# Performance work log

Measured on AMD Instinct MI355X. Metric: run time of the kernel, lower is better.

## Reference

```python
import jax, jax.numpy as jnp
import numpy as np

EMB = 64
N_LEFT = 100000   # m: rows of left_features, b
N_RIGHT = 100000  # n: rows of right_features, c
N_EDGES = 3200000


def setup_inputs() -> dict:
    key = jax.random.key(0)
    ks = jax.random.split(key, 12)
    inp = {
        "left_features": jax.random.normal(ks[0], (N_LEFT, EMB), jnp.float32),
        "right_features_k": jax.random.normal(ks[1], (N_RIGHT, EMB), jnp.float32),
        "edge_index": jax.random.randint(ks[2], (N_EDGES, 2), 0, N_RIGHT, jnp.int64),
        "edge_weight": jax.random.uniform(ks[3], (N_EDGES,), jnp.float32),
        "right_features": jax.random.normal(ks[4], (N_RIGHT, EMB), jnp.float32),
        "c": jax.random.normal(ks[5], (N_RIGHT, 1), jnp.float32),
        "b": jax.random.normal(ks[6], (N_LEFT, 1), jnp.float32),
        # learned parameters
        "temp": jnp.full((2,), 0.9, jnp.float32),
        "W1": jax.random.normal(ks[7], (EMB, EMB), jnp.float32) * 0.05,
        "b1": jnp.zeros((EMB,), jnp.float32),
        "W2": jax.random.normal(ks[8], (EMB, EMB), jnp.float32) * 0.05,
        "b2": jnp.zeros((EMB,), jnp.float32),
    }
    return inp


def reference(left_features, right_features_k, edge_index, edge_weight,
              right_features, c, b, temp, W1, b1, W2, b2):
    # right_to_left=False branch of BipartiteGraphConvolution.forward
    n = right_features.shape[0]  # = c.shape[0]
    # Source quirk: values.sum(dim=-1) on a 1-D vector is a GLOBAL scalar sum,
    # clamped to min 1; every edge weight is scaled by 1/that scalar.
    total = jnp.maximum(jnp.sum(edge_weight), 1.0)
    vals = edge_weight / total                                    # [E]
    row = edge_index[:, 0]  # destination (right) node, in [0, n)
    col = edge_index[:, 1]  # source (left) node, in [0, m)
    # sparse-dense matmul: conv_output = A @ left_features, A in COO (coalesce
    # just sums duplicate entries, identical to segment-sum over raw edges)
    msg = left_features[col] * vals[:, None]                      # [E, EMB]
    conv_output = jax.ops.segment_sum(msg, row, num_segments=n)   # [n, EMB]
    h = right_features + temp[1] * (c - conv_output)              # [n, EMB]
    # output_module: Linear -> ReLU -> Linear (torch Linear: x @ W.T + b)
    h = jax.nn.relu(h @ W1.T + b1)
    out = h @ W2.T + b2
    return out
```

## Files before the change

kernel.cpp:

```cpp
#include <hip/hip_runtime.h>

#define EMB 64
#define BROWS 512
#define BSHIFT 9
#define CHUNK 4096
#define COLBITS 23
#define COLMASK ((1u << COLBITS) - 1u)

__device__ __forceinline__ unsigned short f2bf(float f) {
    unsigned u = __float_as_uint(f);
    u = u + 0x7FFFu + ((u >> 16) & 1u);
    return (unsigned short)(u >> 16);
}

__global__ void convert_left_kernel(const float* __restrict__ left,
                                    unsigned* __restrict__ left16, int n2) {
    int i = blockIdx.x * blockDim.x + threadIdx.x;
    if (i >= n2) return;
    float2 v = ((const float2*)left)[i];
    left16[i] = (unsigned)f2bf(v.x) | ((unsigned)f2bf(v.y) << 16);
}

__global__ void init_bcur_kernel(int* __restrict__ bcur, int nb, int slot) {
    int t = threadIdx.x;
    if (t < nb) bcur[t] = t * slot;
}

__global__ __launch_bounds__(256) void partition_kernel(
    const int2* __restrict__ eidx, const float* __restrict__ w, int n_edges,
    int* __restrict__ bcursor, int2* __restrict__ bsorted,
    float* __restrict__ total) {
    __shared__ int lh[256];
    __shared__ int lo[256];
    __shared__ int go[256];
    __shared__ int lcur[256];
    __shared__ int2 stage[CHUNK];
    __shared__ int dstg[CHUNK];
    int t = threadIdx.x;
    int base = blockIdx.x * CHUNK;
    int cnt = min(CHUNK, n_edges - base);

    lh[t] = 0;
    __syncthreads();
    #pragma unroll
    for (int k = 0; k < CHUNK / 256; ++k) {
        int e = base + t + k * 256;
        if (e < n_edges) atomicAdd(&lh[eidx[e].x >> BSHIFT], 1);
    }
    __syncthreads();
    int v = lh[t];
    lo[t] = v;
    __syncthreads();
    for (int off = 1; off < 256; off <<= 1) {
        int u = (t >= off) ? lo[t - off] : 0;
        __syncthreads();
        lo[t] += u;
        __syncthreads();
    }
    int excl = lo[t] - v;
    go[t] = (v > 0) ? atomicAdd(&bcursor[t], v) : 0;
    __syncthreads();
    lo[t] = excl;
    lcur[t] = excl;
    __syncthreads();

    float s = 0.f;
    #pragma unroll
    for (int k = 0; k < CHUNK / 256; ++k) {
        int e = base + t + k * 256;
        if (e < n_edges) {
            int2 rc = eidx[e];
            float wv = w[e];
            s += wv;
            int b = rc.x >> BSHIFT;
            unsigned rl = (unsigned)(rc.x & (BROWS - 1));
            int p = atomicAdd(&lcur[b], 1);
            stage[p] = make_int2((int)((rl << COLBITS) | (unsigned)rc.y),
                                 __float_as_int(wv));
            dstg[p] = go[b] + (p - lo[b]);
        }
    }
    #pragma unroll
    for (int off = 32; off > 0; off >>= 1) s += __shfl_down(s, off, 64);
    if ((t & 63) == 0) atomicAdd(total, s);
    __syncthreads();
    #pragma unroll
    for (int k = 0; k < CHUNK / 256; ++k) {
        int s2 = t + k * 256;
        if (s2 < cnt) bsorted[dstg[s2]] = stage[s2];
    }
}

__global__ __launch_bounds__(256, 1) void count_scan_kernel(
    const int* __restrict__ bcur, int* __restrict__ sbase, int nb, int slot) {
    __shared__ int ssc[256];
    int t = threadIdx.x;
    int cnt = (t < nb) ? (bcur[t] - t * slot) : 0;
    ssc[t] = cnt;
    __syncthreads();
    for (int off = 1; off < 256; off <<= 1) {
        int u = (t >= off) ? ssc[t - off] : 0;
        __syncthreads();
        ssc[t] += u;
        __syncthreads();
    }
    if (t < nb) sbase[t] = ssc[t] - cnt;
}

__global__ __launch_bounds__(256) void local_rowsort_kernel(
    const int2* __restrict__ bsorted, const int* __restrict__ bcur,
    const int* __restrict__ sbase, int* __restrict__ offs,
    int2* __restrict__ sorted2, int n_right, int slot) {
    __shared__ int lhist[BROWS];
    __shared__ int lcur[BROWS];
    __shared__ int ps[256];
    int b = blockIdx.x;
    int t = threadIdx.x;
    int src0 = b * slot;
    int send = min(bcur[b], src0 + slot);
    int dbase = sbase[b];
    int row0 = b << BSHIFT;
    int nrows = min(BROWS, n_right - row0);

    lhist[2 * t] = 0;
    lhist[2 * t + 1] = 0;
    __syncthreads();
    for (int e = src0 + t; e < send; e += 256)
        atomicAdd(&lhist[((unsigned)bsorted[e].x) >> COLBITS], 1);
    __syncthreads();

    int v0 = lhist[2 * t];
    int v1 = lhist[2 * t + 1];
    int pv = v0 + v1;
    ps[t] = pv;
    __syncthreads();
    for (int off = 1; off < 256; off <<= 1) {
        int u = (t >= off) ? ps[t - off] : 0;
        __syncthreads();
        ps[t] += u;
        __syncthreads();
    }
    int epair = ps[t] - pv;
    lcur[2 * t] = epair;
    lcur[2 * t + 1] = epair + v0;
    if (2 * t < nrows)     offs[row0 + 2 * t]     = dbase + epair;
    if (2 * t + 1 < nrows) offs[row0 + 2 * t + 1] = dbase + epair + v0;
    __syncthreads();

    int e = src0 + t;
    for (; e + 3 * 256 < send; e += 4 * 256) {
        int2 e0 = bsorted[e + 0 * 256];
        int2 e1 = bsorted[e + 1 * 256];
        int2 e2 = bsorted[e + 2 * 256];
        int2 e3 = bsorted[e + 3 * 256];
        int p0 = atomicAdd(&lcur[((unsigned)e0.x) >> COLBITS], 1);
        int p1 = atomicAdd(&lcur[((unsigned)e1.x) >> COLBITS], 1);
        int p2 = atomicAdd(&lcur[((unsigned)e2.x) >> COLBITS], 1);
        int p3 = atomicAdd(&lcur[((unsigned)e3.x) >> COLBITS], 1);
        sorted2[dbase + p0] = e0;
        sorted2[dbase + p1] = e1;
        sorted2[dbase + p2] = e2;
        sorted2[dbase + p3] = e3;
    }
    for (; e < send; e += 256) {
        int2 e0 = bsorted[e];
        int p0 = atomicAdd(&lcur[((unsigned)e0.x) >> COLBITS], 1);
        sorted2[dbase + p0] = e0;
    }
}

__global__ void seg_gather_bf16_kernel(const int2* __restrict__ sorted,
                                       const int* __restrict__ offs,
                                       const uint4* __restrict__ left16o,
                                       const float* __restrict__ right,
                                       const float* __restrict__ c,
                                       const float* __restrict__ temp,
                                       const float* __restrict__ total,
                                       float* __restrict__ hout, int n_right,
                                       int n_edges, int offs_are_ends) {
    int gid = blockIdx.x * blockDim.x + threadIdx.x;
    int wid = gid >> 6;
    int lane = gid & 63;
    if (wid >= n_right) return;
    int start, end;
    if (offs_are_ends) {
        end = offs[wid];
        start = (wid == 0) ? 0 : offs[wid - 1];
    } else {
        start = offs[wid];
        end = (wid + 1 < n_right) ? offs[wid + 1] : n_edges;
    }

    int sub = lane >> 3;
    int d8  = lane & 7;

    float cv = c[wid];
    float inv = 1.0f / fmaxf(total[0], 1.0f);
    float t1 = temp[1];

    float a0 = 0.f, a1 = 0.f, a2 = 0.f, a3 = 0.f;
    float a4 = 0.f, a5 = 0.f, a6 = 0.f, a7 = 0.f;

    if (start < end) {
        int ee = start + sub;
        int2 sv = sorted[(ee < end) ? ee : (end - 1)];
        for (int base = start; base < end; base += 8) {
            int2 cur = sv;
            int ecur = base + sub;
            int bnext = base + 8;
            if (bnext < end) {
                int en = bnext + sub;
                sv = sorted[(en < end) ? en : (end - 1)];
            }
            float wv = (ecur < end) ? __int_as_float(cur.y) : 0.f;
            unsigned col = (unsigned)cur.x & COLMASK;
            uint4 pk = left16o[(size_t)col * 8 + d8];
            a0 = fmaf(wv, __uint_as_float(pk.x << 16), a0);
            a1 = fmaf(wv, __uint_as_float(pk.x & 0xffff0000u), a1);
            a2 = fmaf(wv, __uint_as_float(pk.y << 16), a2);
            a3 = fmaf(wv, __uint_as_float(pk.y & 0xffff0000u), a3);
            a4 = fmaf(wv, __uint_as_float(pk.z << 16), a4);
            a5 = fmaf(wv, __uint_as_float(pk.z & 0xffff0000u), a5);
            a6 = fmaf(wv, __uint_as_float(pk.w << 16), a6);
            a7 = fmaf(wv, __uint_as_float(pk.w & 0xffff0000u), a7);
        }
    }

    #define RED8(x) x += __shfl_xor(x, 8, 64); x += __shfl_xor(x, 16, 64); \
                    x += __shfl_xor(x, 32, 64);
    RED8(a0) RED8(a1) RED8(a2) RED8(a3) RED8(a4) RED8(a5) RED8(a6) RED8(a7)
    #undef RED8

    if (lane < 8) {
        const float4* rp = (const float4*)(right + (size_t)wid * EMB);
        float4 r0 = rp[2 * lane];
        float4 r1 = rp[2 * lane + 1];
        float4 h0, h1;
        h0.x = r0.x + t1 * (cv - a0 * inv);
        h0.y = r0.y + t1 * (cv - a1 * inv);
        h0.z = r0.z + t1 * (cv - a2 * inv);
        h0.w = r0.w + t1 * (cv - a3 * inv);
        h1.x = r1.x + t1 * (cv - a4 * inv);
        h1.y = r1.y + t1 * (cv - a5 * inv);
        h1.z = r1.z + t1 * (cv - a6 * inv);
        h1.w = r1.w + t1 * (cv - a7 * inv);
        float4* op = (float4*)(hout + (size_t)wid * EMB);
        op[2 * lane] = h0;
        op[2 * lane + 1] = h1;
    }
}

__global__ __launch_bounds__(256, 1) void mlp_kernel(
    const float* __restrict__ W1, const float* __restrict__ b1,
    const float* __restrict__ W2, const float* __restrict__ b2,
    float* __restrict__ io, int n) {
    int r = blockIdx.x * blockDim.x + threadIdx.x;
    if (r >= n) return;

    float h[EMB];
    const float4* qp = (const float4*)(io + (size_t)r * EMB);
    #pragma unroll
    for (int q = 0; q < EMB / 4; ++q) {
        float4 qv = qp[q];
        h[4 * q + 0] = qv.x;
        h[4 * q + 1] = qv.y;
        h[4 * q + 2] = qv.z;
        h[4 * q + 3] = qv.w;
    }

    float h1[EMB];
    #pragma unroll
    for (int j = 0; j < EMB; j += 4) {
        float s0 = b1[j + 0], s1 = b1[j + 1], s2 = b1[j + 2], s3 = b1[j + 3];
        #pragma unroll
        for (int k = 0; k < EMB; ++k) {
            float hk = h[k];
            s0 = fmaf(hk, W1[(j + 0) * EMB + k], s0);
            s1 = fmaf(hk, W1[(j + 1) * EMB + k], s1);
            s2 = fmaf(hk, W1[(j + 2) * EMB + k], s2);
            s3 = fmaf(hk, W1[(j + 3) * EMB + k], s3);
        }
        h1[j + 0] = fmaxf(s0, 0.f);
        h1[j + 1] = fmaxf(s1, 0.f);
        h1[j + 2] = fmaxf(s2, 0.f);
        h1[j + 3] = fmaxf(s3, 0.f);
    }

    float4* op = (float4*)(io + (size_t)r * EMB);
    #pragma unroll
    for (int j = 0; j < EMB; j += 4) {
        float s0 = b2[j + 0], s1 = b2[j + 1], s2 = b2[j + 2], s3 = b2[j + 3];
        #pragma unroll
        for (int k = 0; k < EMB; ++k) {
            float hk = h1[k];
            s0 = fmaf(hk, W2[(j + 0) * EMB + k], s0);
            s1 = fmaf(hk, W2[(j + 1) * EMB + k], s1);
            s2 = fmaf(hk, W2[(j + 2) * EMB + k], s2);
            s3 = fmaf(hk, W2[(j + 3) * EMB + k], s3);
        }
        op[j / 4] = make_float4(s0, s1, s2, s3);
    }
}


__global__ void hist_total_kernel(const int2* __restrict__ eidx,
                                  const float* __restrict__ w, int n_edges,
                                  int* __restrict__ counts,
                                  float* __restrict__ total) {
    int gid = blockIdx.x * blockDim.x + threadIdx.x;
    int stride = gridDim.x * blockDim.x;
    float s = 0.f;
    for (int e = gid; e < n_edges; e += stride) {
        s += w[e];
        atomicAdd(&counts[eidx[e].x], 1);
    }
    #pragma unroll
    for (int off = 32; off > 0; off >>= 1) s += __shfl_down(s, off, 64);
    if ((threadIdx.x & 63) == 0) atomicAdd(total, s);
}

__global__ __launch_bounds__(1024, 1) void scan1_kernel(
    const int* __restrict__ cnt, int* __restrict__ incl,
    int* __restrict__ bsums, int n) {
    __shared__ int s[1024];
    int t = threadIdx.x;
    int i = blockIdx.x * 1024 + t;
    int v = (i < n) ? cnt[i] : 0;
    s[t] = v;
    __syncthreads();
    for (int off = 1; off < 1024; off <<= 1) {
        int u = (t >= off) ? s[t - off] : 0;
        __syncthreads();
        s[t] += u;
        __syncthreads();
    }
    if (i < n) incl[i] = s[t];
    if (t == 1023) bsums[blockIdx.x] = s[t];
}

__global__ __launch_bounds__(256, 1) void scan2_kernel(int* __restrict__ bsums, int nb) {
    __shared__ int s[256];
    int t = threadIdx.x;
    int v = (t < nb) ? bsums[t] : 0;
    s[t] = v;
    __syncthreads();
    for (int off = 1; off < 256; off <<= 1) {
        int u = (t >= off) ? s[t - off] : 0;
        __syncthreads();
        s[t] += u;
        __syncthreads();
    }
    if (t < nb) bsums[t] = s[t] - v;
}

__global__ void scan3_kernel(const int* __restrict__ incl,
                             const int* __restrict__ base,
                             int* __restrict__ offs, int n) {
    int i = blockIdx.x * blockDim.x + threadIdx.x;
    if (i >= n) return;
    offs[i] = (i == 0) ? 0 : incl[i - 1] + base[(i - 1) >> 10];
}

__global__ void scatter_kernel(const int2* __restrict__ eidx,
                               const float* __restrict__ w, int n_edges,
                               int* __restrict__ offs,
                               int2* __restrict__ sorted) {
    int gid = blockIdx.x * blockDim.x + threadIdx.x;
    int stride = gridDim.x * blockDim.x;
    for (int e = gid; e < n_edges; e += stride) {
        int2 rc = eidx[e];
        float v = w[e];
        int pos = atomicAdd(&offs[rc.x], 1);
        sorted[pos] = make_int2(rc.y, __float_as_int(v));
    }
}


__global__ void sum_weights_kernel(const float* __restrict__ w, int n,
                                   float* __restrict__ total) {
    int gid = blockIdx.x * blockDim.x + threadIdx.x;
    int stride = gridDim.x * blockDim.x;
    float s = 0.f;
    for (int i = gid; i < n; i += stride) s += w[i];
    #pragma unroll
    for (int off = 32; off > 0; off >>= 1) s += __shfl_down(s, off, 64);
    if ((threadIdx.x & 63) == 0) atomicAdd(total, s);
}

__global__ void edge_scatter_kernel(const int* __restrict__ idx,
                                    const float* __restrict__ w,
                                    const float* __restrict__ left,
                                    const float* __restrict__ total,
                                    float* __restrict__ conv,
                                    long long n_threads) {
    long long gid = (long long)blockIdx.x * blockDim.x + threadIdx.x;
    if (gid >= n_threads) return;
    int e = (int)(gid >> 6);
    int d = (int)(gid & 63);
    float inv = 1.0f / fmaxf(total[0], 1.0f);
    int row = idx[2 * e];
    int col = idx[2 * e + 1];
    float v = w[e] * inv;
    float msg = left[(size_t)col * EMB + d] * v;
    atomicAdd(&conv[(size_t)row * EMB + d], msg);
}

__global__ __launch_bounds__(256, 1) void fused_mlp_kernel(
    const float* __restrict__ right, const float* __restrict__ c,
    const float* __restrict__ temp,
    const float* __restrict__ W1, const float* __restrict__ b1,
    const float* __restrict__ W2, const float* __restrict__ b2,
    float* __restrict__ io, int n) {
    int r = blockIdx.x * blockDim.x + threadIdx.x;
    if (r >= n) return;
    float t1 = temp[1];
    float cv = c[r];
    float h[EMB];
    const float4* rp = (const float4*)(right + (size_t)r * EMB);
    const float4* qp = (const float4*)(io + (size_t)r * EMB);
    #pragma unroll
    for (int q = 0; q < EMB / 4; ++q) {
        float4 rv = rp[q];
        float4 qv = qp[q];
        h[4 * q + 0] = rv.x + t1 * (cv - qv.x);
        h[4 * q + 1] = rv.y + t1 * (cv - qv.y);
        h[4 * q + 2] = rv.z + t1 * (cv - qv.z);
        h[4 * q + 3] = rv.w + t1 * (cv - qv.w);
    }
    float h1[EMB];
    #pragma unroll
    for (int j = 0; j < EMB; j += 4) {
        float s0 = b1[j], s1 = b1[j + 1], s2 = b1[j + 2], s3 = b1[j + 3];
        #pragma unroll
        for (int k = 0; k < EMB; ++k) {
            float hk = h[k];
            s0 = fmaf(hk, W1[(j + 0) * EMB + k], s0);
            s1 = fmaf(hk, W1[(j + 1) * EMB + k], s1);
            s2 = fmaf(hk, W1[(j + 2) * EMB + k], s2);
            s3 = fmaf(hk, W1[(j + 3) * EMB + k], s3);
        }
        h1[j] = fmaxf(s0, 0.f);
        h1[j + 1] = fmaxf(s1, 0.f);
        h1[j + 2] = fmaxf(s2, 0.f);
        h1[j + 3] = fmaxf(s3, 0.f);
    }
    float4* op = (float4*)(io + (size_t)r * EMB);
    #pragma unroll
    for (int j = 0; j < EMB; j += 4) {
        float s0 = b2[j], s1 = b2[j + 1], s2 = b2[j + 2], s3 = b2[j + 3];
        #pragma unroll
        for (int k = 0; k < EMB; ++k) {
            float hk = h1[k];
            s0 = fmaf(hk, W2[(j + 0) * EMB + k], s0);
            s1 = fmaf(hk, W2[(j + 1) * EMB + k], s1);
            s2 = fmaf(hk, W2[(j + 2) * EMB + k], s2);
            s3 = fmaf(hk, W2[(j + 3) * EMB + k], s3);
        }
        op[j / 4] = make_float4(s0, s1, s2, s3);
    }
}


extern "C" void kernel_launch(void* const* d_in, const int* in_sizes, int n_in,
                              void* d_out, int out_size, void* d_ws, size_t ws_size,
                              hipStream_t stream) {
    const float* left   = (const float*)d_in[0];
    const int*   eidx   = (const int*)d_in[2];
    const float* ew     = (const float*)d_in[3];
    const float* right  = (const float*)d_in[4];
    const float* c      = (const float*)d_in[5];
    const float* temp   = (const float*)d_in[7];
    const float* W1     = (const float*)d_in[8];
    const float* b1     = (const float*)d_in[9];
    const float* W2     = (const float*)d_in[10];
    const float* b2     = (const float*)d_in[11];

    const int n_edges = in_sizes[3];
    const int n_right = in_sizes[4] / EMB;
    const int n_left  = in_sizes[0] / EMB;
    float* out = (float*)d_out;

    const int nb = (n_right + BROWS - 1) >> BSHIFT;
    const int nblocks_scan = (n_right + 1023) / 1024;

    auto align256 = [](size_t x) { return (x + 255) & ~(size_t)255; };

    int slot = n_edges / (nb > 0 ? nb : 1);
    slot += slot / 16 + 128;

    size_t off_bcur    = 64;
    size_t off_sbase   = align256(off_bcur + (size_t)nb * 4);
    size_t off_offs    = align256(off_sbase + (size_t)(nb + 1) * 4);
    size_t off_bsorted = align256(off_offs + (size_t)n_right * 4);
    size_t off_sorted2 = align256(off_bsorted + ((size_t)nb * slot + slot) * 8);
    size_t off_left16f = align256(off_sorted2 + (size_t)n_edges * 8);
    size_t req_full    = off_left16f + (size_t)n_left * EMB * 2;

    size_t m_off_offs   = 64;
    size_t m_off_incl   = align256(m_off_offs + (size_t)n_right * 4);
    size_t m_off_bsum   = align256(m_off_incl + (size_t)n_right * 4);
    size_t m_off_sorted = align256(m_off_bsum + 1024);
    size_t m_off_left16 = align256(m_off_sorted + (size_t)n_edges * 8);
    size_t req_mid      = m_off_left16 + (size_t)n_left * EMB * 2;

    bool common_ok = (nb <= 256) && (nblocks_scan <= 256) &&
                     (n_left <= (1 << COLBITS)) && (BROWS * nb >= n_right);

    if (common_ok && ws_size >= req_full) {
        char* ws = (char*)d_ws;
        float* total = (float*)ws;
        int* bcur = (int*)(ws + off_bcur);
        int* sbase = (int*)(ws + off_sbase);
        int* offs = (int*)(ws + off_offs);
        int2* bsorted = (int2*)(ws + off_bsorted);
        int2* sorted2 = (int2*)(ws + off_sorted2);
        unsigned short* left16 = (unsigned short*)(ws + off_left16f);

        hipMemsetAsync(ws, 0, 64, stream);

        int n2 = n_left * EMB / 2;
        convert_left_kernel<<<(n2 + 255) / 256, 256, 0, stream>>>(
            left, (unsigned*)left16, n2);
        init_bcur_kernel<<<1, 256, 0, stream>>>(bcur, nb, slot);
        {
            int nchunks = (n_edges + CHUNK - 1) / CHUNK;
            partition_kernel<<<nchunks, 256, 0, stream>>>(
                (const int2*)eidx, ew, n_edges, bcur, bsorted, total);
        }
        count_scan_kernel<<<1, 256, 0, stream>>>(bcur, sbase, nb, slot);
        local_rowsort_kernel<<<nb, 256, 0, stream>>>(bsorted, bcur, sbase, offs,
                                                     sorted2, n_right, slot);
        {
            long long n_threads = (long long)n_right * EMB;
            int blocks = (int)((n_threads + 255) / 256);
            seg_gather_bf16_kernel<<<blocks, 256, 0, stream>>>(
                sorted2, offs, (const uint4*)left16, right, c, temp, total,
                out, n_right, n_edges, 0);
        }
        mlp_kernel<<<(n_right + 255) / 256, 256, 0, stream>>>(W1, b1, W2, b2,
                                                              out, n_right);
    } else if (common_ok && ws_size >= req_mid) {
        char* ws = (char*)d_ws;
        float* total = (float*)ws;
        int* offs = (int*)(ws + m_off_offs);
        int* incl = (int*)(ws + m_off_incl);
        int* bsum = (int*)(ws + m_off_bsum);
        int2* sorted = (int2*)(ws + m_off_sorted);
        unsigned short* left16 = (unsigned short*)(ws + m_off_left16);

        hipMemsetAsync(ws, 0, m_off_offs + (size_t)n_right * 4, stream);

        int n2 = n_left * EMB / 2;
        convert_left_kernel<<<(n2 + 255) / 256, 256, 0, stream>>>(
            left, (unsigned*)left16, n2);
        hist_total_kernel<<<2048, 256, 0, stream>>>((const int2*)eidx, ew,
                                                    n_edges, offs, total);
        scan1_kernel<<<nblocks_scan, 1024, 0, stream>>>(offs, incl, bsum, n_right);
        scan2_kernel<<<1, 256, 0, stream>>>(bsum, nblocks_scan);
        scan3_kernel<<<(n_right + 255) / 256, 256, 0, stream>>>(incl, bsum, offs,
                                                                n_right);
        scatter_kernel<<<2048, 256, 0, stream>>>((const int2*)eidx, ew, n_edges,
                                                 offs, sorted);
        {
            long long n_threads = (long long)n_right * EMB;
            int blocks = (int)((n_threads + 255) / 256);
            seg_gather_bf16_kernel<<<blocks, 256, 0, stream>>>(
                sorted, offs, (const uint4*)left16, right, c, temp, total,
                out, n_right, n_edges, 1);
        }
        mlp_kernel<<<(n_right + 255) / 256, 256, 0, stream>>>(W1, b1, W2, b2,
                                                              out, n_right);
    } else {
        float* total = (float*)d_ws;
        hipMemsetAsync(d_out, 0, (size_t)out_size * sizeof(float), stream);
        hipMemsetAsync(d_ws, 0, sizeof(float), stream);
        sum_weights_kernel<<<2048, 256, 0, stream>>>(ew, n_edges, total);
        long long n_threads = (long long)n_edges * EMB;
        long long blocks = (n_threads + 255) / 256;
        edge_scatter_kernel<<<(int)blocks, 256, 0, stream>>>(
            eidx, ew, left, total, out, n_threads);
        int mblocks = (n_right + 255) / 256;
        fused_mlp_kernel<<<mblocks, 256, 0, stream>>>(right, c, temp, W1, b1, W2,
                                                      b2, out, n_right);
    }
}
```

Before: 279.4 us.

## Restructure MLP kernel to tile 64 rows per block via shared memory

```diff
diff --git a/kernel.cpp b/kernel.cpp
--- a/kernel.cpp
+++ b/kernel.cpp
@@ -6,6 +6,8 @@
 #define CHUNK 4096
 #define COLBITS 23
 #define COLMASK ((1u << COLBITS) - 1u)
+#define MROWS 64
+#define HPAD 66
 
 __device__ __forceinline__ unsigned short f2bf(float f) {
     unsigned u = __float_as_uint(f);
@@ -250,55 +252,59 @@
     }
 }
 
-__global__ __launch_bounds__(256, 1) void mlp_kernel(
+__global__ __launch_bounds__(256, 4) void mlp_kernel(
     const float* __restrict__ W1, const float* __restrict__ b1,
     const float* __restrict__ W2, const float* __restrict__ b2,
     float* __restrict__ io, int n) {
-    int r = blockIdx.x * blockDim.x + threadIdx.x;
-    if (r >= n) return;
-
-    float h[EMB];
-    const float4* qp = (const float4*)(io + (size_t)r * EMB);
-    #pragma unroll
-    for (int q = 0; q < EMB / 4; ++q) {
-        float4 qv = qp[q];
-        h[4 * q + 0] = qv.x;
-        h[4 * q + 1] = qv.y;
-        h[4 * q + 2] = qv.z;
-        h[4 * q + 3] = qv.w;
-    }
-
-    float h1[EMB];
-    #pragma unroll
-    for (int j = 0; j < EMB; j += 4) {
-        float s0 = b1[j + 0], s1 = b1[j + 1], s2 = b1[j + 2], s3 = b1[j + 3];
+    __shared__ float hT[64 * HPAD];
+    __shared__ float h1T[64 * 64];
+    int t = threadIdx.x;
+    int r = t & 63;
+    int q = __builtin_amdgcn_readfirstlane(t >> 6);
+    int row0 = blockIdx.x * MROWS;
+
+    #pragma unroll
+    for (int i = 0; i < 16; ++i) {
+        int rr = i * 4 + q;
+        int gr = row0 + rr;
+        float v = (gr < n) ? io[(size_t)gr * EMB + r] : 0.f;
+        hT[r * HPAD + rr] = v;
+    }
+    __syncthreads();
+
+    float acc[16];
+    #pragma unroll
+    for (int jj = 0; jj < 16; ++jj) acc[jj] = b1[q * 16 + jj];
+    for (int k = 0; k < 64; ++k) {
+        float hk = hT[k * HPAD + r];
         #pragma unroll
-        for (int k = 0; k < EMB; ++k) {
-            float hk = h[k];
-            s0 = fmaf(hk, W1[(j + 0) * EMB + k], s0);
-            s1 = fmaf(hk, W1[(j + 1) * EMB + k], s1);
-            s2 = fmaf(hk, W1[(j + 2) * EMB + k], s2);
-            s3 = fmaf(hk, W1[(j + 3) * EMB + k], s3);
-        }
-        h1[j + 0] = fmaxf(s0, 0.f);
-        h1[j + 1] = fmaxf(s1, 0.f);
-        h1[j + 2] = fmaxf(s2, 0.f);
-        h1[j + 3] = fmaxf(s3, 0.f);
-    }
-
-    float4* op = (float4*)(io + (size_t)r * EMB);
-    #pragma unroll
-    for (int j = 0; j < EMB; j += 4) {
-        float s0 = b2[j + 0], s1 = b2[j + 1], s2 = b2[j + 2], s3 = b2[j + 3];
+        for (int jj = 0; jj < 16; ++jj)
+            acc[jj] = fmaf(hk, W1[(q * 16 + jj) * EMB + k], acc[jj]);
+    }
+    #pragma unroll
+    for (int jj = 0; jj < 16; ++jj)
+        h1T[(q * 16 + jj) * 64 + r] = fmaxf(acc[jj], 0.f);
+    __syncthreads();
+
+    #pragma unroll
+    for (int jj = 0; jj < 16; ++jj) acc[jj] = b2[q * 16 + jj];
+    for (int k = 0; k < 64; ++k) {
+        float hk = h1T[k * 64 + r];
         #pragma unroll
-        for (int k = 0; k < EMB; ++k) {
-            float hk = h1[k];
-            s0 = fmaf(hk, W2[(j + 0) * EMB + k], s0);
-            s1 = fmaf(hk, W2[(j + 1) * EMB + k], s1);
-            s2 = fmaf(hk, W2[(j + 2) * EMB + k], s2);
-            s3 = fmaf(hk, W2[(j + 3) * EMB + k], s3);
-        }
-        op[j / 4] = make_float4(s0, s1, s2, s3);
+        for (int jj = 0; jj < 16; ++jj)
+            acc[jj] = fmaf(hk, W2[(q * 16 + jj) * EMB + k], acc[jj]);
+    }
+    __syncthreads();
+    #pragma unroll
+    for (int jj = 0; jj < 16; ++jj)
+        hT[(q * 16 + jj) * HPAD + r] = acc[jj];
+    __syncthreads();
+
+    #pragma unroll
+    for (int i = 0; i < 16; ++i) {
+        int rr = i * 4 + q;
+        int gr = row0 + rr;
+        if (gr < n) io[(size_t)gr * EMB + r] = hT[r * HPAD + rr];
     }
 }
 
@@ -419,13 +425,13 @@
     const float4* rp = (const float4*)(right + (size_t)r * EMB);
     const float4* qp = (const float4*)(io + (size_t)r * EMB);
     #pragma unroll
-    for (int q = 0; q < EMB / 4; ++q) {
-        float4 rv = rp[q];
-        float4 qv = qp[q];
-        h[4 * q + 0] = rv.x + t1 * (cv - qv.x);
-        h[4 * q + 1] = rv.y + t1 * (cv - qv.y);
-        h[4 * q + 2] = rv.z + t1 * (cv - qv.z);
-        h[4 * q + 3] = rv.w + t1 * (cv - qv.w);
+    for (int qq = 0; qq < EMB / 4; ++qq) {
+        float4 rv = rp[qq];
+        float4 qv = qp[qq];
+        h[4 * qq + 0] = rv.x + t1 * (cv - qv.x);
+        h[4 * qq + 1] = rv.y + t1 * (cv - qv.y);
+        h[4 * qq + 2] = rv.z + t1 * (cv - qv.z);
+        h[4 * qq + 3] = rv.w + t1 * (cv - qv.w);
     }
     float h1[EMB];
     #pragma unroll
@@ -537,8 +543,8 @@
                 sorted2, offs, (const uint4*)left16, right, c, temp, total,
                 out, n_right, n_edges, 0);
         }
-        mlp_kernel<<<(n_right + 255) / 256, 256, 0, stream>>>(W1, b1, W2, b2,
-                                                              out, n_right);
+        mlp_kernel<<<(n_right + MROWS - 1) / MROWS, 256, 0, stream>>>(
+            W1, b1, W2, b2, out, n_right);
     } else if (common_ok && ws_size >= req_mid) {
         char* ws = (char*)d_ws;
         float* total = (float*)ws;
@@ -568,8 +574,8 @@
                 sorted, offs, (const uint4*)left16, right, c, temp, total,
                 out, n_right, n_edges, 1);
         }
-        mlp_kernel<<<(n_right + 255) / 256, 256, 0, stream>>>(W1, b1, W2, b2,
-                                                              out, n_right);
+        mlp_kernel<<<(n_right + MROWS - 1) / MROWS, 256, 0, stream>>>(
+            W1, b1, W2, b2, out, n_right);
     } else {
         float* total = (float*)d_ws;
         hipMemsetAsync(d_out, 0, (size_t)out_size * sizeof(float), stream);
```

Result: faster. 255.4 us (-8.6%).
